# Kernel tuning notes

Hardware: AMD Instinct MI355X
Metric: run time of the kernel (lower is better)

The kernel has to match this reference:

```python
import jax, jax.numpy as jnp
import numpy as np

B, L, D, H = 64, 1024, 256, 256


def setup_inputs() -> dict:
    key = jax.random.key(0)
    ks = jax.random.split(key, 10)
    s = 0.05  # small init to keep tanh/sigmoid in linear-ish range
    return {
        "x":  jax.random.normal(ks[0], (B, L, D), jnp.float32),
        # LSTM cell params (keras gate order i, f, g, o)
        "Wk": jax.random.normal(ks[1], (D, 4 * H), jnp.float32) * s,
        "Wr": jax.random.normal(ks[2], (H, 4 * H), jnp.float32) * s,
        "b":  jnp.zeros((4 * H,), jnp.float32),
        # Attention params
        "W1": jax.random.normal(ks[3], (D, H), jnp.float32) * s,
        "b1": jnp.zeros((H,), jnp.float32),
        "W2": jax.random.normal(ks[4], (H, H), jnp.float32) * s,
        "b2": jnp.zeros((H,), jnp.float32),
        "V":  jax.random.normal(ks[5], (H, 1), jnp.float32) * s,
        "bV": jnp.zeros((1,), jnp.float32),
    }


def reference(x, Wk, Wr, b, W1, b1, W2, b2, V, bV):
    Bb, Ll, Dd = x.shape
    Hh = Wr.shape[0]
    # Encoder projection, computed once (W1 @ encoder_outputs)
    w1_e = jnp.einsum('bld,dh->blh', x, W1) + b1            # (B, L, H)
    # Decoder input is the last encoder step, repeated every step
    x_in = x[:, -1, :]                                      # (B, D)
    xz = x_in @ Wk + b                                      # (B, 4H), constant per step
    h0 = jnp.zeros((Bb, Hh), x.dtype)
    c0 = jnp.zeros((Bb, Hh), x.dtype)

    def step(carry, _):
        h, c = carry
        z = xz + h @ Wr                                     # (B, 4H)
        i, f, g, o = jnp.split(z, 4, axis=-1)
        i = jax.nn.sigmoid(i)
        f = jax.nn.sigmoid(f)
        g = jnp.tanh(g)
        o = jax.nn.sigmoid(o)
        c = f * c + i * g
        h = o * jnp.tanh(c)
        # Additive (Bahdanau) attention: v^T tanh(W1 e + W2 d)
        w2_d = (h @ W2 + b2)[:, None, :]                    # (B, 1, H)
        scores = jnp.tanh(w1_e + w2_d) @ V + bV             # (B, L, 1)
        attn = jax.nn.softmax(scores[..., 0], axis=1)       # (B, L)
        return (h, c), attn

    _, attn_seq = jax.lax.scan(step, (h0, c0), None, length=Ll)  # (L, B, L)
    return jnp.transpose(attn_seq, (1, 0, 2))               # (B, L_steps, L_ptr)
```

## Files before the change

### kernel.cpp

```cpp
#include <hip/hip_runtime.h>
#include <hip/hip_bf16.h>


#define LOG2E  1.4426950408889634f
#define C2LOG2E 2.8853900817779268f

typedef float f32x2 __attribute__((ext_vector_type(2)));

__device__ __forceinline__ unsigned f2bf(float f) {
  unsigned u = __builtin_bit_cast(unsigned, f);
  return (u + 0x7fffu + ((u >> 16) & 1u)) >> 16;
}
__device__ __forceinline__ float bfbits2f(unsigned bits) {
  return __builtin_bit_cast(float, bits << 16);
}
__device__ __forceinline__ float bfhi2f(unsigned bits) {
  return __builtin_bit_cast(float, bits & 0xffff0000u);
}

#if defined(__has_builtin)
#  if __has_builtin(__builtin_amdgcn_fdot2_f32_bf16)
#    define HAS_DOT2_BF16 1
#  endif
#endif

#if defined(HAS_DOT2_BF16)
typedef __bf16 bf16x2v __attribute__((ext_vector_type(2)));
__device__ __forceinline__ float dot2bf(unsigned w, unsigned h, float acc) {
  return __builtin_amdgcn_fdot2_f32_bf16(__builtin_bit_cast(bf16x2v, w),
                                         __builtin_bit_cast(bf16x2v, h), acc, false);
}
#else
__device__ __forceinline__ float dot2bf(unsigned w, unsigned h, float acc) {
  float wl = __builtin_bit_cast(float, w << 16);
  float wh = __builtin_bit_cast(float, w & 0xffff0000u);
  float hl = __builtin_bit_cast(float, h << 16);
  float hh = __builtin_bit_cast(float, h & 0xffff0000u);
  return fmaf(wh, hh, fmaf(wl, hl, acc));
}
#endif

#if defined(__has_builtin) && __has_builtin(__builtin_amdgcn_rcpf)
#  define FAST_RCP(x) __builtin_amdgcn_rcpf(x)
#else
#  define FAST_RCP(x) (1.0f / (x))
#endif

__device__ __forceinline__ float fast_sigmoid(float x) {
  return FAST_RCP(1.f + exp2f(-LOG2E * x));
}
__device__ __forceinline__ float fast_tanh(float x) {
  return 1.f - 2.f * FAST_RCP(1.f + exp2f(C2LOG2E * x));
}

__global__ __launch_bounds__(256) void k1_w1e(const float* __restrict__ x,
                                              const float* __restrict__ W1,
                                              const float* __restrict__ b1,
                                              uint2* __restrict__ ATq) {
  __shared__ unsigned short tile[256 * 16];
  const int b  = blockIdx.x >> 6;
  const int lb = blockIdx.x & 63;
  const int h  = threadIdx.x;
  float acc[16];
  const float bias = b1[h];
#pragma unroll
  for (int r = 0; r < 16; ++r) acc[r] = bias;
  const float* xb = x + ((size_t)(b * 1024 + lb * 16)) * 256;
  for (int d0 = 0; d0 < 256; d0 += 4) {
    const float w0 = W1[(d0 + 0) * 256 + h];
    const float w1 = W1[(d0 + 1) * 256 + h];
    const float w2 = W1[(d0 + 2) * 256 + h];
    const float w3 = W1[(d0 + 3) * 256 + h];
#pragma unroll
    for (int r = 0; r < 16; ++r) {
      const float4 xv = *(const float4*)(xb + r * 256 + d0);
      acc[r] = fmaf(xv.x, w0, acc[r]);
      acc[r] = fmaf(xv.y, w1, acc[r]);
      acc[r] = fmaf(xv.z, w2, acc[r]);
      acc[r] = fmaf(xv.w, w3, acc[r]);
    }
  }
#pragma unroll
  for (int r = 0; r < 16; ++r)
    tile[h * 16 + r] = (unsigned short)f2bf(exp2f(C2LOG2E * acc[r]));
  __syncthreads();
#pragma unroll
  for (int k = 0; k < 4; ++k) {
    const int o = k * 256 + threadIdx.x;
    const int hq = o >> 4, lloc = o & 15;
    const unsigned s0 = tile[(4 * hq + 0) * 16 + lloc];
    const unsigned s1 = tile[(4 * hq + 1) * 16 + lloc];
    const unsigned s2 = tile[(4 * hq + 2) * 16 + lloc];
    const unsigned s3 = tile[(4 * hq + 3) * 16 + lloc];
    uint2 val;
    val.x = s0 | (s1 << 16);
    val.y = s2 | (s3 << 16);
    ATq[(((size_t)(b * 64 + hq)) << 10) + lb * 16 + lloc] = val;
  }
}

__global__ __launch_bounds__(256) void k2_xz(const float* __restrict__ x,
                                             const float* __restrict__ Wk,
                                             const float* __restrict__ bvec,
                                             float* __restrict__ xz) {
  const int b = blockIdx.x, tid = threadIdx.x;
  float acc[4] = {bvec[tid], bvec[256 + tid], bvec[512 + tid], bvec[768 + tid]};
  const float* xr = x + ((size_t)b * 1024 + 1023) * 256;
  for (int d0 = 0; d0 < 256; d0 += 4) {
    const float4 xv = *(const float4*)(xr + d0);
#pragma unroll
    for (int i = 0; i < 4; ++i) {
      const float xs = (i == 0) ? xv.x : (i == 1) ? xv.y : (i == 2) ? xv.z : xv.w;
#pragma unroll
      for (int q = 0; q < 4; ++q)
        acc[q] = fmaf(xs, Wk[(size_t)(d0 + i) * 1024 + q * 256 + tid], acc[q]);
    }
  }
#pragma unroll
  for (int q = 0; q < 4; ++q) xz[b * 1024 + q * 256 + tid] = acc[q];
}

__global__ __launch_bounds__(512, 2) void k3_recur(const float* __restrict__ xz,
                                                   const float* __restrict__ Wr,
                                                   unsigned short* __restrict__ hseq) {
  __shared__ __align__(16) unsigned Wtail[8 * 1024 * 4];
  __shared__ float z_lds[512];
  __shared__ __align__(16) unsigned h_pk[128];
  const int b   = blockIdx.x;
  const int tid = threadIdx.x;
  const int colA = tid, colB = tid + 512;

  unsigned wA[96], wB[96];
#pragma unroll
  for (int p = 0; p < 96; ++p) {
    wA[p] = f2bf(Wr[(size_t)(2 * p) * 1024 + colA]) |
            (f2bf(Wr[(size_t)(2 * p + 1) * 1024 + colA]) << 16);
    wB[p] = f2bf(Wr[(size_t)(2 * p) * 1024 + colB]) |
            (f2bf(Wr[(size_t)(2 * p + 1) * 1024 + colB]) << 16);
  }
#pragma unroll
  for (int gg = 0; gg < 8; ++gg) {
#pragma unroll
    for (int d = 0; d < 4; ++d) {
      const int p = 96 + gg * 4 + d;
      Wtail[(gg * 1024 + colA) * 4 + d] =
          f2bf(Wr[(size_t)(2 * p) * 1024 + colA]) |
          (f2bf(Wr[(size_t)(2 * p + 1) * 1024 + colA]) << 16);
      Wtail[(gg * 1024 + colB) * 4 + d] =
          f2bf(Wr[(size_t)(2 * p) * 1024 + colB]) |
          (f2bf(Wr[(size_t)(2 * p + 1) * 1024 + colB]) << 16);
    }
  }
  if (tid < 128) h_pk[tid] = 0u;
  const float zaA = xz[b * 1024 + colA];
  const float zaB = xz[b * 1024 + colB];
  float c = 0.f;
  __syncthreads();

  for (int t = 0; t < 1024; ++t) {
    float aA0 = zaA, aA1 = 0.f, aB0 = zaB, aB1 = 0.f;
#pragma unroll
    for (int g = 0; g < 12; ++g) {
      const uint4 hp = *(const uint4*)&h_pk[4 * g];
      aA0 = dot2bf(wA[4 * g + 0], hp.x, aA0);
      aA0 = dot2bf(wA[4 * g + 1], hp.y, aA0);
      aA0 = dot2bf(wA[4 * g + 2], hp.z, aA0);
      aA0 = dot2bf(wA[4 * g + 3], hp.w, aA0);
      aB0 = dot2bf(wB[4 * g + 0], hp.x, aB0);
      aB0 = dot2bf(wB[4 * g + 1], hp.y, aB0);
      aB0 = dot2bf(wB[4 * g + 2], hp.z, aB0);
      aB0 = dot2bf(wB[4 * g + 3], hp.w, aB0);
    }
#pragma unroll
    for (int g = 12; g < 24; ++g) {
      const uint4 hp = *(const uint4*)&h_pk[4 * g];
      aA1 = dot2bf(wA[4 * g + 0], hp.x, aA1);
      aA1 = dot2bf(wA[4 * g + 1], hp.y, aA1);
      aA1 = dot2bf(wA[4 * g + 2], hp.z, aA1);
      aA1 = dot2bf(wA[4 * g + 3], hp.w, aA1);
      aB1 = dot2bf(wB[4 * g + 0], hp.x, aB1);
      aB1 = dot2bf(wB[4 * g + 1], hp.y, aB1);
      aB1 = dot2bf(wB[4 * g + 2], hp.z, aB1);
      aB1 = dot2bf(wB[4 * g + 3], hp.w, aB1);
    }
#pragma unroll
    for (int gg = 0; gg < 8; ++gg) {
      const uint4 hp = *(const uint4*)&h_pk[96 + 4 * gg];
      const uint4 wa = *(const uint4*)&Wtail[(gg * 1024 + colA) * 4];
      const uint4 wb = *(const uint4*)&Wtail[(gg * 1024 + colB) * 4];
      float& rA = (gg < 4) ? aA0 : aA1;
      float& rB = (gg < 4) ? aB0 : aB1;
      rA = dot2bf(wa.x, hp.x, rA);
      rA = dot2bf(wa.y, hp.y, rA);
      rA = dot2bf(wa.z, hp.z, rA);
      rA = dot2bf(wa.w, hp.w, rA);
      rB = dot2bf(wb.x, hp.x, rB);
      rB = dot2bf(wb.y, hp.y, rB);
      rB = dot2bf(wb.z, hp.z, rB);
      rB = dot2bf(wb.w, hp.w, rB);
    }
    const float aA = aA0 + aA1;
    const float aB = aB0 + aB1;
    if (tid >= 256) {
      z_lds[tid - 256] = aA;
      z_lds[tid]       = aB;
    }
    __syncthreads();
    if (tid < 256) {
      const float zi = aA;
      const float zg = aB;
      const float zf = z_lds[tid];
      const float zo = z_lds[tid + 256];
      const float ig = fast_sigmoid(zi);
      const float fg = fast_sigmoid(zf);
      const float gv = fast_tanh(zg);
      const float og = fast_sigmoid(zo);
      c = fmaf(fg, c, ig * gv);
      const float h = og * fast_tanh(c);
      const unsigned short hb = (unsigned short)f2bf(h);
      ((unsigned short*)h_pk)[tid] = hb;
      hseq[(size_t)(t * 64 + b) * 256 + tid] = hb;
    }
    __syncthreads();
  }
}

__global__ __launch_bounds__(256) void k3b_w2d(const unsigned int* __restrict__ hseq,
                                               const float* __restrict__ W2,
                                               const float* __restrict__ b2,
                                               float* __restrict__ D) {
  const int r0 = blockIdx.x * 16;
  const int h = threadIdx.x;
  float acc[16];
  const float bias = b2[h];
#pragma unroll
  for (int r = 0; r < 16; ++r) acc[r] = bias;
  for (int m0 = 0; m0 < 128; m0 += 2) {
    const float w0 = W2[(size_t)(2 * m0 + 0) * 256 + h];
    const float w1 = W2[(size_t)(2 * m0 + 1) * 256 + h];
    const float w2 = W2[(size_t)(2 * m0 + 2) * 256 + h];
    const float w3 = W2[(size_t)(2 * m0 + 3) * 256 + h];
#pragma unroll
    for (int r = 0; r < 16; ++r) {
      const uint2 hp = *(const uint2*)&hseq[(size_t)(r0 + r) * 128 + m0];
      acc[r] = fmaf(bfbits2f(hp.x),       w0, acc[r]);
      acc[r] = fmaf(bfbits2f(hp.x >> 16), w1, acc[r]);
      acc[r] = fmaf(bfbits2f(hp.y),       w2, acc[r]);
      acc[r] = fmaf(bfbits2f(hp.y >> 16), w3, acc[r]);
    }
  }
  const int t = r0 >> 6;
  const int bb0 = r0 & 63;
#pragma unroll
  for (int r = 0; r < 16; ++r) {
    D[((size_t)(bb0 + r) * 1024 + t) * 256 + h] = exp2f(C2LOG2E * acc[r]);
  }
}

__global__ __launch_bounds__(256, 3) void k4_attn(const uint2* __restrict__ ATq,
                                                  const float* __restrict__ Dm,
                                                  const float* __restrict__ V,
                                                  float* __restrict__ out) {
  const int b  = blockIdx.x >> 6;
  const int tb = blockIdx.x & 63;
  const int wv = threadIdx.x >> 6;
  const int lane = threadIdx.x & 63;
  const int t0 = tb * 16 + wv * 4;
  const uint2* Ab = ATq + (((size_t)b) << 16);
  const float* Db = Dm + ((size_t)(b * 1024) + t0) * 256;
  f32x2 acc2[2][16];
#pragma unroll
  for (int p = 0; p < 2; ++p)
#pragma unroll
    for (int lb = 0; lb < 16; ++lb) acc2[p][lb] = (f32x2){0.f, 0.f};

  for (int hq = 0; hq < 64; ++hq) {
    const float4 vq  = *(const float4*)(V + hq * 4);
    const float4 Dr0 = *(const float4*)(Db + 0 * 256 + hq * 4);
    const float4 Dr1 = *(const float4*)(Db + 1 * 256 + hq * 4);
    const float4 Dr2 = *(const float4*)(Db + 2 * 256 + hq * 4);
    const float4 Dr3 = *(const float4*)(Db + 3 * 256 + hq * 4);
    f32x2 Dp[2][4];
    Dp[0][0] = (f32x2){Dr0.x, Dr1.x}; Dp[0][1] = (f32x2){Dr0.y, Dr1.y};
    Dp[0][2] = (f32x2){Dr0.z, Dr1.z}; Dp[0][3] = (f32x2){Dr0.w, Dr1.w};
    Dp[1][0] = (f32x2){Dr2.x, Dr3.x}; Dp[1][1] = (f32x2){Dr2.y, Dr3.y};
    Dp[1][2] = (f32x2){Dr2.z, Dr3.z}; Dp[1][3] = (f32x2){Dr2.w, Dr3.w};
    const f32x2 v0 = (f32x2){vq.x, vq.x};
    const f32x2 v1 = (f32x2){vq.y, vq.y};
    const f32x2 v2 = (f32x2){vq.z, vq.z};
    const f32x2 v3 = (f32x2){vq.w, vq.w};
    const uint2* Ah = Ab + ((size_t)hq << 10) + lane;
#pragma unroll
    for (int lb = 0; lb < 16; ++lb) {
      const uint2 aq = Ah[lb * 64];
      const f32x2 a0 = (f32x2){bfbits2f(aq.x), bfbits2f(aq.x)};
      const f32x2 a1 = (f32x2){bfhi2f(aq.x),   bfhi2f(aq.x)};
      const f32x2 a2 = (f32x2){bfbits2f(aq.y), bfbits2f(aq.y)};
      const f32x2 a3 = (f32x2){bfhi2f(aq.y),   bfhi2f(aq.y)};
      const f32x2 one = (f32x2){1.f, 1.f};
#pragma unroll
      for (int p = 0; p < 2; ++p) {
        const f32x2 d0 = a0 * Dp[p][0] + one;
        const f32x2 d1 = a1 * Dp[p][1] + one;
        const f32x2 d2 = a2 * Dp[p][2] + one;
        const f32x2 d3 = a3 * Dp[p][3] + one;
        const f32x2 n01 = v0 * d1 + v1 * d0;
        const f32x2 n23 = v2 * d3 + v3 * d2;
        const f32x2 d01 = d0 * d1;
        const f32x2 d23 = d2 * d3;
        const f32x2 nf = n01 * d23 + n23 * d01;
        const f32x2 df = d01 * d23;
        const f32x2 r = (f32x2){FAST_RCP(df.x), FAST_RCP(df.y)};
        acc2[p][lb] += nf * r;
      }
    }
  }
#pragma unroll
  for (int p = 0; p < 2; ++p)
#pragma unroll
    for (int half = 0; half < 2; ++half) {
      const int tt = 2 * p + half;
      float s[16];
      float m = -1e30f;
#pragma unroll
      for (int lb = 0; lb < 16; ++lb) {
        s[lb] = -2.f * (half ? acc2[p][lb].y : acc2[p][lb].x);
        m = fmaxf(m, s[lb]);
      }
      for (int off = 32; off > 0; off >>= 1) m = fmaxf(m, __shfl_xor(m, off, 64));
      float pr[16];
      float sum = 0.f;
#pragma unroll
      for (int lb = 0; lb < 16; ++lb) {
        pr[lb] = exp2f((s[lb] - m) * LOG2E);
        sum += pr[lb];
      }
      for (int off = 32; off > 0; off >>= 1) sum += __shfl_xor(sum, off, 64);
      const float rs = 1.f / sum;
      float* op = out + ((size_t)(b * 1024) + (t0 + tt)) * 1024 + lane;
#pragma unroll
      for (int lb = 0; lb < 16; ++lb) op[lb * 64] = pr[lb] * rs;
    }
}

extern "C" void kernel_launch(void* const* d_in, const int* in_sizes, int n_in,
                              void* d_out, int out_size, void* d_ws, size_t ws_size,
                              hipStream_t stream) {
  (void)in_sizes; (void)n_in; (void)out_size; (void)ws_size;
  const float* x  = (const float*)d_in[0];
  const float* Wk = (const float*)d_in[1];
  const float* Wr = (const float*)d_in[2];
  const float* bb = (const float*)d_in[3];
  const float* W1 = (const float*)d_in[4];
  const float* b1 = (const float*)d_in[5];
  const float* W2 = (const float*)d_in[6];
  const float* b2 = (const float*)d_in[7];
  const float* V  = (const float*)d_in[8];

  char* ws = (char*)d_ws;
  float*          Dm   = (float*)(ws);
  uint2*          ATq  = (uint2*)(ws + 67108864);
  unsigned short* hseq = (unsigned short*)(ws + 100663296);
  float*          xz   = (float*)(ws + 134217728);
  float* out = (float*)d_out;

  hipLaunchKernelGGL(k1_w1e, dim3(4096), dim3(256), 0, stream, x, W1, b1, ATq);
  hipLaunchKernelGGL(k2_xz, dim3(64), dim3(256), 0, stream, x, Wk, bb, xz);
  hipLaunchKernelGGL(k3_recur, dim3(64), dim3(512), 0, stream, xz, Wr, hseq);
  hipLaunchKernelGGL(k3b_w2d, dim3(4096), dim3(256), 0, stream, (const unsigned int*)hseq, W2, b2, Dm);
  hipLaunchKernelGGL(k4_attn, dim3(4096), dim3(256), 0, stream, ATq, Dm, V, out);
}
```

Before: 4.166 ms.

## Overlap encoder projection with LSTM recurrence in one fused launch

Merges the W1·x encoder projection kernel into the recurrence kernel as extra blocks, so the 64 sequential LSTM blocks share the GPU with 4096 projection blocks that fill the otherwise idle compute units. The projection blocks now use 512 threads, each handling 8 rows. Every block reserves the recurrence kernel's large shared-memory footprint, which can limit how many projection blocks fit per CU. The recurrence loop's __syncthreads is also replaced with a raw lgkmcnt wait plus s_barrier to cut barrier overhead.

```diff
diff --git a/kernel.cpp b/kernel.cpp
--- a/kernel.cpp
+++ b/kernel.cpp
@@ -17,6 +17,12 @@
 __device__ __forceinline__ float bfhi2f(unsigned bits) {
   return __builtin_bit_cast(float, bits & 0xffff0000u);
 }
+
+#define CHEAP_BAR()                                            \
+  do {                                                         \
+    asm volatile("s_waitcnt lgkmcnt(0)\n\ts_barrier" ::: "memory"); \
+    __builtin_amdgcn_sched_barrier(0);                         \
+  } while (0)
 
 #if defined(__has_builtin)
 #  if __has_builtin(__builtin_amdgcn_fdot2_f32_bf16)
@@ -51,52 +57,6 @@
 }
 __device__ __forceinline__ float fast_tanh(float x) {
   return 1.f - 2.f * FAST_RCP(1.f + exp2f(C2LOG2E * x));
-}
-
-__global__ __launch_bounds__(256) void k1_w1e(const float* __restrict__ x,
-                                              const float* __restrict__ W1,
-                                              const float* __restrict__ b1,
-                                              uint2* __restrict__ ATq) {
-  __shared__ unsigned short tile[256 * 16];
-  const int b  = blockIdx.x >> 6;
-  const int lb = blockIdx.x & 63;
-  const int h  = threadIdx.x;
-  float acc[16];
-  const float bias = b1[h];
-#pragma unroll
-  for (int r = 0; r < 16; ++r) acc[r] = bias;
-  const float* xb = x + ((size_t)(b * 1024 + lb * 16)) * 256;
-  for (int d0 = 0; d0 < 256; d0 += 4) {
-    const float w0 = W1[(d0 + 0) * 256 + h];
-    const float w1 = W1[(d0 + 1) * 256 + h];
-    const float w2 = W1[(d0 + 2) * 256 + h];
-    const float w3 = W1[(d0 + 3) * 256 + h];
-#pragma unroll
-    for (int r = 0; r < 16; ++r) {
-      const float4 xv = *(const float4*)(xb + r * 256 + d0);
-      acc[r] = fmaf(xv.x, w0, acc[r]);
-      acc[r] = fmaf(xv.y, w1, acc[r]);
-      acc[r] = fmaf(xv.z, w2, acc[r]);
-      acc[r] = fmaf(xv.w, w3, acc[r]);
-    }
-  }
-#pragma unroll
-  for (int r = 0; r < 16; ++r)
-    tile[h * 16 + r] = (unsigned short)f2bf(exp2f(C2LOG2E * acc[r]));
-  __syncthreads();
-#pragma unroll
-  for (int k = 0; k < 4; ++k) {
-    const int o = k * 256 + threadIdx.x;
-    const int hq = o >> 4, lloc = o & 15;
-    const unsigned s0 = tile[(4 * hq + 0) * 16 + lloc];
-    const unsigned s1 = tile[(4 * hq + 1) * 16 + lloc];
-    const unsigned s2 = tile[(4 * hq + 2) * 16 + lloc];
-    const unsigned s3 = tile[(4 * hq + 3) * 16 + lloc];
-    uint2 val;
-    val.x = s0 | (s1 << 16);
-    val.y = s2 | (s3 << 16);
-    ATq[(((size_t)(b * 64 + hq)) << 10) + lb * 16 + lloc] = val;
-  }
 }
 
 __global__ __launch_bounds__(256) void k2_xz(const float* __restrict__ x,
@@ -120,108 +80,158 @@
   for (int q = 0; q < 4; ++q) xz[b * 1024 + q * 256 + tid] = acc[q];
 }
 
-__global__ __launch_bounds__(512, 2) void k3_recur(const float* __restrict__ xz,
-                                                   const float* __restrict__ Wr,
-                                                   unsigned short* __restrict__ hseq) {
-  __shared__ __align__(16) unsigned Wtail[8 * 1024 * 4];
-  __shared__ float z_lds[512];
-  __shared__ __align__(16) unsigned h_pk[128];
-  const int b   = blockIdx.x;
+__global__ __launch_bounds__(512, 2) void k3_fat(const float* __restrict__ xz,
+                                                 const float* __restrict__ Wr,
+                                                 unsigned short* __restrict__ hseq,
+                                                 const float* __restrict__ x,
+                                                 const float* __restrict__ W1,
+                                                 const float* __restrict__ b1,
+                                                 uint2* __restrict__ ATq) {
+  __shared__ __align__(16) unsigned smem[8 * 1024 * 4 + 512 + 128];
   const int tid = threadIdx.x;
-  const int colA = tid, colB = tid + 512;
-
-  unsigned wA[96], wB[96];
-#pragma unroll
-  for (int p = 0; p < 96; ++p) {
-    wA[p] = f2bf(Wr[(size_t)(2 * p) * 1024 + colA]) |
+  if (blockIdx.x < 64) {
+    unsigned* Wtail = smem;
+    float*    z_lds = (float*)(smem + 32768);
+    unsigned* h_pk  = smem + 32768 + 512;
+    const int b = blockIdx.x;
+    const int colA = tid, colB = tid + 512;
+
+    unsigned wA[96], wB[96];
+#pragma unroll
+    for (int p = 0; p < 96; ++p) {
+      wA[p] = f2bf(Wr[(size_t)(2 * p) * 1024 + colA]) |
+              (f2bf(Wr[(size_t)(2 * p + 1) * 1024 + colA]) << 16);
+      wB[p] = f2bf(Wr[(size_t)(2 * p) * 1024 + colB]) |
+              (f2bf(Wr[(size_t)(2 * p + 1) * 1024 + colB]) << 16);
+    }
+#pragma unroll
+    for (int gg = 0; gg < 8; ++gg) {
+#pragma unroll
+      for (int d = 0; d < 4; ++d) {
+        const int p = 96 + gg * 4 + d;
+        Wtail[(gg * 1024 + colA) * 4 + d] =
+            f2bf(Wr[(size_t)(2 * p) * 1024 + colA]) |
             (f2bf(Wr[(size_t)(2 * p + 1) * 1024 + colA]) << 16);
-    wB[p] = f2bf(Wr[(size_t)(2 * p) * 1024 + colB]) |
+        Wtail[(gg * 1024 + colB) * 4 + d] =
+            f2bf(Wr[(size_t)(2 * p) * 1024 + colB]) |
             (f2bf(Wr[(size_t)(2 * p + 1) * 1024 + colB]) << 16);
-  }
-#pragma unroll
-  for (int gg = 0; gg < 8; ++gg) {
-#pragma unroll
-    for (int d = 0; d < 4; ++d) {
-      const int p = 96 + gg * 4 + d;
-      Wtail[(gg * 1024 + colA) * 4 + d] =
-          f2bf(Wr[(size_t)(2 * p) * 1024 + colA]) |
-          (f2bf(Wr[(size_t)(2 * p + 1) * 1024 + colA]) << 16);
-      Wtail[(gg * 1024 + colB) * 4 + d] =
-          f2bf(Wr[(size_t)(2 * p) * 1024 + colB]) |
-          (f2bf(Wr[(size_t)(2 * p + 1) * 1024 + colB]) << 16);
-    }
-  }
-  if (tid < 128) h_pk[tid] = 0u;
-  const float zaA = xz[b * 1024 + colA];
-  const float zaB = xz[b * 1024 + colB];
-  float c = 0.f;
-  __syncthreads();
-
-  for (int t = 0; t < 1024; ++t) {
-    float aA0 = zaA, aA1 = 0.f, aB0 = zaB, aB1 = 0.f;
-#pragma unroll
-    for (int g = 0; g < 12; ++g) {
-      const uint4 hp = *(const uint4*)&h_pk[4 * g];
-      aA0 = dot2bf(wA[4 * g + 0], hp.x, aA0);
-      aA0 = dot2bf(wA[4 * g + 1], hp.y, aA0);
-      aA0 = dot2bf(wA[4 * g + 2], hp.z, aA0);
-      aA0 = dot2bf(wA[4 * g + 3], hp.w, aA0);
-      aB0 = dot2bf(wB[4 * g + 0], hp.x, aB0);
-      aB0 = dot2bf(wB[4 * g + 1], hp.y, aB0);
-      aB0 = dot2bf(wB[4 * g + 2], hp.z, aB0);
-      aB0 = dot2bf(wB[4 * g + 3], hp.w, aB0);
-    }
-#pragma unroll
-    for (int g = 12; g < 24; ++g) {
-      const uint4 hp = *(const uint4*)&h_pk[4 * g];
-      aA1 = dot2bf(wA[4 * g + 0], hp.x, aA1);
-      aA1 = dot2bf(wA[4 * g + 1], hp.y, aA1);
-      aA1 = dot2bf(wA[4 * g + 2], hp.z, aA1);
-      aA1 = dot2bf(wA[4 * g + 3], hp.w, aA1);
-      aB1 = dot2bf(wB[4 * g + 0], hp.x, aB1);
-      aB1 = dot2bf(wB[4 * g + 1], hp.y, aB1);
-      aB1 = dot2bf(wB[4 * g + 2], hp.z, aB1);
-      aB1 = dot2bf(wB[4 * g + 3], hp.w, aB1);
-    }
-#pragma unroll
-    for (int gg = 0; gg < 8; ++gg) {
-      const uint4 hp = *(const uint4*)&h_pk[96 + 4 * gg];
-      const uint4 wa = *(const uint4*)&Wtail[(gg * 1024 + colA) * 4];
-      const uint4 wb = *(const uint4*)&Wtail[(gg * 1024 + colB) * 4];
-      float& rA = (gg < 4) ? aA0 : aA1;
-      float& rB = (gg < 4) ? aB0 : aB1;
-      rA = dot2bf(wa.x, hp.x, rA);
-      rA = dot2bf(wa.y, hp.y, rA);
-      rA = dot2bf(wa.z, hp.z, rA);
-      rA = dot2bf(wa.w, hp.w, rA);
-      rB = dot2bf(wb.x, hp.x, rB);
-      rB = dot2bf(wb.y, hp.y, rB);
-      rB = dot2bf(wb.z, hp.z, rB);
-      rB = dot2bf(wb.w, hp.w, rB);
-    }
-    const float aA = aA0 + aA1;
-    const float aB = aB0 + aB1;
-    if (tid >= 256) {
-      z_lds[tid - 256] = aA;
-      z_lds[tid]       = aB;
-    }
+      }
+    }
+    if (tid < 128) h_pk[tid] = 0u;
+    const float zaA = xz[b * 1024 + colA];
+    const float zaB = xz[b * 1024 + colB];
+    float c = 0.f;
+    CHEAP_BAR();
+
+    for (int t = 0; t < 1024; ++t) {
+      float aA0 = zaA, aA1 = 0.f, aB0 = zaB, aB1 = 0.f;
+#pragma unroll
+      for (int g = 0; g < 12; ++g) {
+        const uint4 hp = *(const uint4*)&h_pk[4 * g];
+        aA0 = dot2bf(wA[4 * g + 0], hp.x, aA0);
+        aA0 = dot2bf(wA[4 * g + 1], hp.y, aA0);
+        aA0 = dot2bf(wA[4 * g + 2], hp.z, aA0);
+        aA0 = dot2bf(wA[4 * g + 3], hp.w, aA0);
+        aB0 = dot2bf(wB[4 * g + 0], hp.x, aB0);
+        aB0 = dot2bf(wB[4 * g + 1], hp.y, aB0);
+        aB0 = dot2bf(wB[4 * g + 2], hp.z, aB0);
+        aB0 = dot2bf(wB[4 * g + 3], hp.w, aB0);
+      }
+#pragma unroll
+      for (int g = 12; g < 24; ++g) {
+        const uint4 hp = *(const uint4*)&h_pk[4 * g];
+        aA1 = dot2bf(wA[4 * g + 0], hp.x, aA1);
+        aA1 = dot2bf(wA[4 * g + 1], hp.y, aA1);
+        aA1 = dot2bf(wA[4 * g + 2], hp.z, aA1);
+        aA1 = dot2bf(wA[4 * g + 3], hp.w, aA1);
+        aB1 = dot2bf(wB[4 * g + 0], hp.x, aB1);
+        aB1 = dot2bf(wB[4 * g + 1], hp.y, aB1);
+        aB1 = dot2bf(wB[4 * g + 2], hp.z, aB1);
+        aB1 = dot2bf(wB[4 * g + 3], hp.w, aB1);
+      }
+#pragma unroll
+      for (int gg = 0; gg < 8; ++gg) {
+        const uint4 hp = *(const uint4*)&h_pk[96 + 4 * gg];
+        const uint4 wa = *(const uint4*)&Wtail[(gg * 1024 + colA) * 4];
+        const uint4 wb = *(const uint4*)&Wtail[(gg * 1024 + colB) * 4];
+        float& rA = (gg < 4) ? aA0 : aA1;
+        float& rB = (gg < 4) ? aB0 : aB1;
+        rA = dot2bf(wa.x, hp.x, rA);
+        rA = dot2bf(wa.y, hp.y, rA);
+        rA = dot2bf(wa.z, hp.z, rA);
+        rA = dot2bf(wa.w, hp.w, rA);
+        rB = dot2bf(wb.x, hp.x, rB);
+        rB = dot2bf(wb.y, hp.y, rB);
+        rB = dot2bf(wb.z, hp.z, rB);
+        rB = dot2bf(wb.w, hp.w, rB);
+      }
+      const float aA = aA0 + aA1;
+      const float aB = aB0 + aB1;
+      if (tid >= 256) {
+        z_lds[tid - 256] = aA;
+        z_lds[tid]       = aB;
+      }
+      CHEAP_BAR();
+      if (tid < 256) {
+        const float zi = aA;
+        const float zg = aB;
+        const float zf = z_lds[tid];
+        const float zo = z_lds[tid + 256];
+        const float ig = fast_sigmoid(zi);
+        const float fg = fast_sigmoid(zf);
+        const float gv = fast_tanh(zg);
+        const float og = fast_sigmoid(zo);
+        c = fmaf(fg, c, ig * gv);
+        const float h = og * fast_tanh(c);
+        const unsigned short hb = (unsigned short)f2bf(h);
+        ((unsigned short*)h_pk)[tid] = hb;
+        hseq[(size_t)(t * 64 + b) * 256 + tid] = hb;
+      }
+      CHEAP_BAR();
+    }
+  } else {
+    unsigned short* tile = (unsigned short*)smem;
+    const int bid = blockIdx.x - 64;
+    const int b  = bid >> 6;
+    const int lb = bid & 63;
+    const int h    = tid & 255;
+    const int half = tid >> 8;
+    float acc[8];
+    const float bias = b1[h];
+#pragma unroll
+    for (int r = 0; r < 8; ++r) acc[r] = bias;
+    const float* xb = x + ((size_t)(b * 1024 + lb * 16 + half * 8)) * 256;
+    for (int d0 = 0; d0 < 256; d0 += 4) {
+      const float w0 = W1[(d0 + 0) * 256 + h];
+      const float w1 = W1[(d0 + 1) * 256 + h];
+      const float w2 = W1[(d0 + 2) * 256 + h];
+      const float w3 = W1[(d0 + 3) * 256 + h];
+#pragma unroll
+      for (int r = 0; r < 8; ++r) {
+        const float4 xv = *(const float4*)(xb + r * 256 + d0);
+        acc[r] = fmaf(xv.x, w0, acc[r]);
+        acc[r] = fmaf(xv.y, w1, acc[r]);
+        acc[r] = fmaf(xv.z, w2, acc[r]);
+        acc[r] = fmaf(xv.w, w3, acc[r]);
+      }
+    }
+#pragma unroll
+    for (int r = 0; r < 8; ++r)
+      tile[h * 16 + half * 8 + r] = (unsigned short)f2bf(exp2f(C2LOG2E * acc[r]));
     __syncthreads();
-    if (tid < 256) {
-      const float zi = aA;
-      const float zg = aB;
-      const float zf = z_lds[tid];
-      const float zo = z_lds[tid + 256];
-      const float ig = fast_sigmoid(zi);
-      const float fg = fast_sigmoid(zf);
-      const float gv = fast_tanh(zg);
-      const float og = fast_sigmoid(zo);
-      c = fmaf(fg, c, ig * gv);
-      const float h = og * fast_tanh(c);
-      const unsigned short hb = (unsigned short)f2bf(h);
-      ((unsigned short*)h_pk)[tid] = hb;
-      hseq[(size_t)(t * 64 + b) * 256 + tid] = hb;
-    }
-    __syncthreads();
+#pragma unroll
+    for (int k = 0; k < 2; ++k) {
+      const int o = k * 512 + tid;
+      const int hq = o >> 4, lloc = o & 15;
+      const unsigned s0 = tile[(4 * hq + 0) * 16 + lloc];
+      const unsigned s1 = tile[(4 * hq + 1) * 16 + lloc];
+      const unsigned s2 = tile[(4 * hq + 2) * 16 + lloc];
+      const unsigned s3 = tile[(4 * hq + 3) * 16 + lloc];
+      uint2 val;
+      val.x = s0 | (s1 << 16);
+      val.y = s2 | (s3 << 16);
+      ATq[(((size_t)(b * 64 + hq)) << 10) + lb * 16 + lloc] = val;
+    }
   }
 }
 
@@ -364,9 +374,10 @@
   float*          xz   = (float*)(ws + 134217728);
   float* out = (float*)d_out;
 
-  hipLaunchKernelGGL(k1_w1e, dim3(4096), dim3(256), 0, stream, x, W1, b1, ATq);
   hipLaunchKernelGGL(k2_xz, dim3(64), dim3(256), 0, stream, x, Wk, bb, xz);
-  hipLaunchKernelGGL(k3_recur, dim3(64), dim3(512), 0, stream, xz, Wr, hseq);
-  hipLaunchKernelGGL(k3b_w2d, dim3(4096), dim3(256), 0, stream, (const unsigned int*)hseq, W2, b2, Dm);
+  hipLaunchKernelGGL(k3_fat, dim3(64 + 4096), dim3(512), 0, stream,
+                     xz, Wr, hseq, x, W1, b1, ATq);
+  hipLaunchKernelGGL(k3b_w2d, dim3(4096), dim3(256), 0, stream,
+                     (const unsigned int*)hseq, W2, b2, Dm);
   hipLaunchKernelGGL(k4_attn, dim3(4096), dim3(256), 0, stream, ATq, Dm, V, out);
 }
```

Measured after the change: 4.201 ms. Within noise of the previous version (+0.8%).
